# Kernel optimization log

Measured on AMD Instinct MI355X. Metric: run time of the kernel, lower is better.

## Reference

```python
import jax, jax.numpy as jnp
import numpy as np

N_STEPS = 20
ALPHA, BETA = 0.9, 0.8  # synaptic / membrane decay (unused given zero carried state, kept for clarity)


def _lcn_spiking_layer(h, knn, w, b):
    """h: [N, d_in]; knn: [d_out, K] indices into d_in; w: [d_out, K]; b: [1, d_out].
    Gather K neighbors per output node, weight, reduce, then snntorch Synaptic
    update with zero carried state (the source never stores returned syn/mem):
      syn = ALPHA*0 + I = I ; reset = (prev_mem > thr) = 0 ; mem = BETA*0 + syn - 0 = I
    and the layer output is mem (the source keeps the 3rd return value)."""
    g = h[:, knn]                                  # [N, d_out, K] irregular gather
    cur = jnp.sum(g * w[None, :, :], axis=2) + b   # [N, d_out]
    syn = ALPHA * jnp.zeros_like(cur) + cur
    mem = BETA * jnp.zeros_like(cur) + syn         # reset term is zero
    return mem


def setup_inputs() -> dict:
    key = jax.random.key(0)
    B, T, IN_DIM, K, OUT = 32, N_STEPS, 14400, 25, 2
    dims = [7200, 3600, 1800, 900, 450]
    ks = jax.random.split(key, 13)
    inp = {"x": jax.random.normal(ks[0], (B, T, IN_DIM), dtype=jnp.float32)}
    prev = IN_DIM
    for i, d in enumerate(dims):
        inp[f"w{i}"] = jax.random.normal(ks[1 + i], (d, K), dtype=jnp.float32) * (2.0 / K) ** 0.5
        inp[f"b{i}"] = jnp.zeros((1, d), dtype=jnp.float32)
        inp[f"knn{i}"] = jax.random.randint(ks[6 + i], (d, K), 0, prev)
        prev = d
    inp["Wfc"] = jax.random.normal(ks[11], (dims[-1], OUT), dtype=jnp.float32) * (1.0 / dims[-1]) ** 0.5
    inp["bfc"] = jnp.zeros((OUT,), dtype=jnp.float32)
    return inp


def reference(x, w0, w1, w2, w3, w4, b0, b1, b2, b3, b4, Wfc, bfc,
              knn0, knn1, knn2, knn3, knn4):
    # Source loops over 20 timesteps with independent (state never carried) work;
    # fold time into batch to vectorize, then keep the last step's angle only,
    # exactly matching the returned value of the torch forward.
    B, T, D = x.shape
    h = x.reshape(B * T, D)
    layers = ((w0, b0, knn0), (w1, b1, knn1), (w2, b2, knn2), (w3, b3, knn3), (w4, b4, knn4))
    for w, b, knn in layers:
        h = _lcn_spiking_layer(h, knn, w, b)
    angle = h @ Wfc + bfc                     # [B*T, out_dim]
    angle = angle.reshape(B, T, -1)[:, -1]    # last timestep, as in the source
    return angle
```

## Files before the change

kernel.cpp:

```cpp
#include <hip/hip_runtime.h>


#define ROWS 32
#define TSTEPS 20
#define D0 14400
#define D1 7200
#define D2 3600
#define D3 1800
#define D4 900
#define D5 450
#define KNB 25

#define GATHER25(acc, kp, wp, SRC)                                  \
    {                                                               \
        _Pragma("unroll")                                           \
        for (int k = 0; k < 24; k += 4) {                           \
            int4   ki; __builtin_memcpy(&ki, (kp) + k, 16);         \
            float4 wi; __builtin_memcpy(&wi, (wp) + k, 16);         \
            acc += SRC(ki.x) * wi.x + SRC(ki.y) * wi.y              \
                 + SRC(ki.z) * wi.z + SRC(ki.w) * wi.w;             \
        }                                                           \
        acc += SRC((kp)[24]) * (wp)[24];                            \
    }

__global__ __launch_bounds__(256)
void l0_stage(const float* __restrict__ x, float* __restrict__ h1t,
              const float* __restrict__ w, const float* __restrict__ bvec,
              const int* __restrict__ knn)
{
    __shared__ float s[D0];
    const int r = blockIdx.y;
    const float* xrow = x + ((size_t)r * TSTEPS + (TSTEPS - 1)) * (size_t)D0;

    const float4* src = reinterpret_cast<const float4*>(xrow);
    float4* dst = reinterpret_cast<float4*>(s);
#pragma unroll 2
    for (int i = threadIdx.x; i < D0 / 4; i += 256)
        dst[i] = src[i];
    __syncthreads();

    const int j0 = blockIdx.x * 900;
#pragma unroll 1
    for (int j = j0 + threadIdx.x; j < j0 + 900; j += 256) {
        const int*   kn = knn + j * KNB;
        const float* ww = w   + j * KNB;
        float acc = bvec[j];
#define LDS_SRC(idx) s[idx]
        GATHER25(acc, kn, ww, LDS_SRC)
#undef LDS_SRC
        h1t[(j << 5) + r] = acc;
    }
}

__global__ __launch_bounds__(256)
void layer_t_k(const float* __restrict__ pin, float* __restrict__ pout,
               const float* __restrict__ w, const float* __restrict__ bvec,
               const int* __restrict__ knn, int npairs)
{
    const int lane = threadIdx.x & 63;
    const int r  = lane & 31;
    const int jj = lane >> 5;
    const int nw = gridDim.x << 2;
#pragma unroll 1
    for (int jp = (blockIdx.x << 2) + (threadIdx.x >> 6); jp < npairs; jp += nw) {
        const int j = (jp << 1) + jj;
        const int*   kn = knn + j * KNB;
        const float* ww = w   + j * KNB;
        float acc = bvec[j];
#pragma unroll
        for (int k = 0; k < KNB; ++k)
            acc += pin[(kn[k] << 5) + r] * ww[k];
        pout[(j << 5) + r] = acc;
    }
}

__global__ __launch_bounds__(256)
void layer_t_k_rm(const float* __restrict__ pin, float* __restrict__ pout,
                  const float* __restrict__ w, const float* __restrict__ bvec,
                  const int* __restrict__ knn, int npairs, int dout)
{
    const int lane = threadIdx.x & 63;
    const int r  = lane & 31;
    const int jj = lane >> 5;
    const int nw = gridDim.x << 2;
#pragma unroll 1
    for (int jp = (blockIdx.x << 2) + (threadIdx.x >> 6); jp < npairs; jp += nw) {
        const int j = (jp << 1) + jj;
        const int*   kn = knn + j * KNB;
        const float* ww = w   + j * KNB;
        float acc = bvec[j];
#pragma unroll
        for (int k = 0; k < KNB; ++k)
            acc += pin[(kn[k] << 5) + r] * ww[k];
        pout[r * dout + j] = acc;
    }
}

__global__ __launch_bounds__(1024)
void tail34fc(const float* __restrict__ h3,
              const float* __restrict__ w3, const float* __restrict__ b3, const int* __restrict__ n3,
              const float* __restrict__ w4, const float* __restrict__ b4, const int* __restrict__ n4,
              const float* __restrict__ Wfc, const float* __restrict__ bfc,
              float* __restrict__ out)
{
    __shared__ float s3[D3];
    __shared__ float s4[D4];
    __shared__ float s5[D5];
    __shared__ float red[2];

    const int r   = blockIdx.x;
    const int tid = threadIdx.x;

    if (tid < D3 / 4) {
        reinterpret_cast<float4*>(s3)[tid] =
            reinterpret_cast<const float4*>(h3 + (size_t)r * D3)[tid];
    }
    if (tid == 0) { red[0] = bfc[0]; red[1] = bfc[1]; }
    __syncthreads();

    if (tid < D4) {
        const int*   kn = n3 + tid * KNB;
        const float* ww = w3 + tid * KNB;
        float acc = b3[tid];
#define S3_SRC(idx) s3[idx]
        GATHER25(acc, kn, ww, S3_SRC)
#undef S3_SRC
        s4[tid] = acc;
    }
    __syncthreads();

    if (tid < D5) {
        const int*   kn = n4 + tid * KNB;
        const float* ww = w4 + tid * KNB;
        float acc = b4[tid];
#define S4_SRC(idx) s4[idx]
        GATHER25(acc, kn, ww, S4_SRC)
#undef S4_SRC
        s5[tid] = acc;
    }
    __syncthreads();

    float c0 = 0.0f, c1 = 0.0f;
    if (tid < D5) {
        const float v = s5[tid];
        c0 = v * Wfc[2 * tid + 0];
        c1 = v * Wfc[2 * tid + 1];
    }
#pragma unroll
    for (int off = 32; off > 0; off >>= 1) {
        c0 += __shfl_down(c0, off);
        c1 += __shfl_down(c1, off);
    }
    if ((tid & 63) == 0 && tid < D5) {
        atomicAdd(&red[0], c0);
        atomicAdd(&red[1], c1);
    }
    __syncthreads();
    if (tid < 2)
        out[2 * r + tid] = red[tid];
}

extern "C" void kernel_launch(void* const* d_in, const int* in_sizes, int n_in,
                              void* d_out, int out_size, void* d_ws, size_t ws_size,
                              hipStream_t stream)
{
    const float* x    = (const float*)d_in[0];
    const float* w0   = (const float*)d_in[1];
    const float* b0   = (const float*)d_in[2];
    const int*   knn0 = (const int*)  d_in[3];
    const float* w1   = (const float*)d_in[4];
    const float* b1   = (const float*)d_in[5];
    const int*   knn1 = (const int*)  d_in[6];
    const float* w2   = (const float*)d_in[7];
    const float* b2   = (const float*)d_in[8];
    const int*   knn2 = (const int*)  d_in[9];
    const float* w3   = (const float*)d_in[10];
    const float* b3   = (const float*)d_in[11];
    const int*   knn3 = (const int*)  d_in[12];
    const float* w4   = (const float*)d_in[13];
    const float* b4   = (const float*)d_in[14];
    const int*   knn4 = (const int*)  d_in[15];
    const float* Wfc  = (const float*)d_in[16];
    const float* bfc  = (const float*)d_in[17];
    float* out = (float*)d_out;

    float* h1t = (float*)d_ws;
    float* h2t = h1t + (size_t)D1 * ROWS;
    float* h3  = h2t + (size_t)D2 * ROWS;

    l0_stage<<<dim3(D1 / 900, ROWS), dim3(256), 0, stream>>>(x, h1t, w0, b0, knn0);

    layer_t_k<<<dim3(450), dim3(256), 0, stream>>>(h1t, h2t, w1, b1, knn1, D2 / 2);

    layer_t_k_rm<<<dim3(225), dim3(256), 0, stream>>>(h2t, h3, w2, b2, knn2, D3 / 2, D3);

    tail34fc<<<dim3(ROWS), dim3(1024), 0, stream>>>(
        h3,
        w3, b3, knn3,
        w4, b4, knn4,
        Wfc, bfc, out);
}
```

Measured before the change: 126.1 us.

## Transpose last-timestep input and reuse transposed gather kernel for layer 0

Replaces the per-row layer-0 kernel, which copied the whole 14400-float input row into LDS and gathered from it, with two kernels. The first transposes the last-timestep input into a [D0][32] layout, and the second reuses the transposed-layout gather kernel, so each gathered neighbor serves all 32 rows with coalesced loads and the knn/weight reads are shared across rows. It also vectorizes the knn and weight loads in the transposed gather loop. The cost is an extra kernel launch and an extra round trip of the input through global memory.

```diff
diff --git a/kernel.cpp b/kernel.cpp
--- a/kernel.cpp
+++ b/kernel.cpp
@@ -23,32 +23,38 @@
         acc += SRC((kp)[24]) * (wp)[24];                            \
     }
 
+#define GATHER25_T(acc, kp, wp, pin, r)                             \
+    {                                                               \
+        _Pragma("unroll")                                           \
+        for (int k = 0; k < 24; k += 4) {                           \
+            int4   ki; __builtin_memcpy(&ki, (kp) + k, 16);         \
+            float4 wi; __builtin_memcpy(&wi, (wp) + k, 16);         \
+            acc += (pin)[(ki.x << 5) + (r)] * wi.x                  \
+                 + (pin)[(ki.y << 5) + (r)] * wi.y                  \
+                 + (pin)[(ki.z << 5) + (r)] * wi.z                  \
+                 + (pin)[(ki.w << 5) + (r)] * wi.w;                 \
+        }                                                           \
+        acc += (pin)[((kp)[24] << 5) + (r)] * (wp)[24];             \
+    }
+
 __global__ __launch_bounds__(256)
-void l0_stage(const float* __restrict__ x, float* __restrict__ h1t,
-              const float* __restrict__ w, const float* __restrict__ bvec,
-              const int* __restrict__ knn)
-{
-    __shared__ float s[D0];
-    const int r = blockIdx.y;
-    const float* xrow = x + ((size_t)r * TSTEPS + (TSTEPS - 1)) * (size_t)D0;
-
-    const float4* src = reinterpret_cast<const float4*>(xrow);
-    float4* dst = reinterpret_cast<float4*>(s);
-#pragma unroll 2
-    for (int i = threadIdx.x; i < D0 / 4; i += 256)
-        dst[i] = src[i];
-    __syncthreads();
-
-    const int j0 = blockIdx.x * 900;
-#pragma unroll 1
-    for (int j = j0 + threadIdx.x; j < j0 + 900; j += 256) {
-        const int*   kn = knn + j * KNB;
-        const float* ww = w   + j * KNB;
-        float acc = bvec[j];
-#define LDS_SRC(idx) s[idx]
-        GATHER25(acc, kn, ww, LDS_SRC)
-#undef LDS_SRC
-        h1t[(j << 5) + r] = acc;
+void xpose(const float* __restrict__ x, float* __restrict__ xT)
+{
+    __shared__ float t[32][33];
+    const int d0 = blockIdx.x << 5;
+    const int c  = threadIdx.x & 31;
+    const int q  = threadIdx.x >> 5;
+
+#pragma unroll
+    for (int i = 0; i < 4; ++i) {
+        const int r = q + (i << 3);
+        t[c][r] = x[(size_t)r * (TSTEPS * D0) + (size_t)(TSTEPS - 1) * D0 + d0 + c];
+    }
+    __syncthreads();
+#pragma unroll
+    for (int i = 0; i < 4; ++i) {
+        const int dd = q + (i << 3);
+        xT[((d0 + dd) << 5) + c] = t[dd][c];
     }
 }
 
@@ -67,9 +73,7 @@
         const int*   kn = knn + j * KNB;
         const float* ww = w   + j * KNB;
         float acc = bvec[j];
-#pragma unroll
-        for (int k = 0; k < KNB; ++k)
-            acc += pin[(kn[k] << 5) + r] * ww[k];
+        GATHER25_T(acc, kn, ww, pin, r)
         pout[(j << 5) + r] = acc;
     }
 }
@@ -89,9 +93,7 @@
         const int*   kn = knn + j * KNB;
         const float* ww = w   + j * KNB;
         float acc = bvec[j];
-#pragma unroll
-        for (int k = 0; k < KNB; ++k)
-            acc += pin[(kn[k] << 5) + r] * ww[k];
+        GATHER25_T(acc, kn, ww, pin, r)
         pout[r * dout + j] = acc;
     }
 }
@@ -184,11 +186,14 @@
     const float* bfc  = (const float*)d_in[17];
     float* out = (float*)d_out;
 
-    float* h1t = (float*)d_ws;
+    float* xT  = (float*)d_ws;
+    float* h1t = xT  + (size_t)D0 * ROWS;
     float* h2t = h1t + (size_t)D1 * ROWS;
     float* h3  = h2t + (size_t)D2 * ROWS;
 
-    l0_stage<<<dim3(D1 / 900, ROWS), dim3(256), 0, stream>>>(x, h1t, w0, b0, knn0);
+    xpose<<<dim3(D0 / 32), dim3(256), 0, stream>>>(x, xT);
+
+    layer_t_k<<<dim3(900), dim3(256), 0, stream>>>(xT, h1t, w0, b0, knn0, D1 / 2);
 
     layer_t_k<<<dim3(450), dim3(256), 0, stream>>>(h1t, h2t, w1, b1, knn1, D2 / 2);
 
```

Result: no change. 128.0 us (+1.5%).
